# Optimization experiments

Hardware: AMD Instinct MI355X
Metric: run time of the kernel (lower is better)

Reference implementation:

```python
import jax, jax.numpy as jnp
import numpy as np

# Transformer config constants (from init_kwargs)
SRF = 3.0                 # spatial_receptive_field
SRF2 = SRF * SRF
ALPHA = 2.0
BETA = 8.0
GAMMA = 16.0
RES = jnp.array([0.5, 0.5, 0.5], dtype=jnp.float32)   # relative_positional_gresolution
N_BUCKETS = 2 * 8 + 1                                  # 2*beta + 1 = 17
MUL = jnp.array([N_BUCKETS ** 2, N_BUCKETS, 1], dtype=jnp.float32)  # [289,17,1]
SLICES_PER_ROT = 2


def setup_inputs() -> dict:
    key = jax.random.key(0)
    k1, k2 = jax.random.split(key)
    N = 3072
    # LiDAR-like point coordinates in a 10m cube; receptive field 3.0 makes radius filter selective
    xyz = jax.random.uniform(k1, (N, 3), dtype=jnp.float32) * 10.0
    # grid columns: [batch, block, gx, gy, gz]; values < 128 per the torch assert
    grid = jax.random.randint(k2, (N, 5), 0, 8, dtype=jnp.int32)
    return {"xyz": xyz, "grid": grid}


def _bucket_base(x):
    # from_dxyz_to_bucket_base, res.size(0)==3 branch
    x = x / RES
    x_abs = jnp.abs(x)
    log_ratio = jnp.log(jnp.maximum(x_abs, 1e-6) / ALPHA) / np.log(GAMMA / ALPHA)
    sup = jnp.minimum(jnp.round(ALPHA - (BETA - ALPHA) * log_ratio), BETA)
    sup = jnp.sign(x) * sup
    return BETA + jnp.where(x_abs <= ALPHA, jnp.round(x), sup)


def reference(xyz, grid):
    # no-kvp path of jit_compute_interactions, expressed as dense [N,N] pair masks
    batch = grid[:, 0]
    block = grid[:, 1]
    coords = grid[:, 2:]            # grid_look[:, 1:]

    # batch equality filter (meshgrid + batch==batch)
    batch_eq = batch[:, None] == batch[None, :]
    # causal block filter: block[iq] <= block[ik]
    block_le = block[:, None] <= block[None, :]

    # force_keep_neighbours: adjacent voxels within the same block
    coord_adj = jnp.max(jnp.abs(coords[:, None, :] - coords[None, :, :]), axis=-1) <= 1
    forcekeep = coord_adj & (block[:, None] == block[None, :])

    # coarse spatial hash on xy: ceil(xy / srf), neighbor cells only
    xy_coarse = jnp.ceil(xyz[:, :2] / SRF).astype(jnp.int32)
    keep_coarse = jnp.max(jnp.abs(xy_coarse[:, None, :] - xy_coarse[None, :, :]), axis=-1) <= 1

    # pairwise deltas (torch uses fp16 here; fp32 kept for numerical clarity) [N,N,3]
    dxyz = xyz[:, None, :] - xyz[None, :, :]
    keepr = jnp.sum(dxyz * dxyz, axis=-1) <= SRF2

    mask = batch_eq & block_le & (forcekeep | keep_coarse) & (forcekeep | keepr)

    dxyz_m = jnp.where(mask[..., None], dxyz, 0.0)

    # from_dxyz_to_bucket_mul: log-bucketize each axis, flatten via mul_buckets
    buckets = jnp.sum(MUL * _bucket_base(dxyz_m), axis=-1).astype(jnp.int32)
    buckets = jnp.where(mask, buckets, 0)

    # dscanid = scanid[ik] - scanid[iq], scanid = block // slices_per_rotation
    scanid = block // SLICES_PER_ROT
    dscanid = jnp.where(mask, scanid[None, :] - scanid[:, None], 0)

    return dxyz_m, buckets, dscanid, mask
```

## Files before the change

### kernel.cpp

```cpp
#include <hip/hip_runtime.h>
#include <cmath>


__device__ __forceinline__ float bucket_base(float v) {
    const float x  = v * 2.0f;
    const float xa = fabsf(x);
    if (xa <= 2.0f) {
        return 8.0f + rintf(x);
    }
    const float lr = logf(fmaxf(xa, 1e-6f) * 0.5f) / 2.0794415416798357f;
    const float sup = fminf(rintf(2.0f - 6.0f * lr), 8.0f);
    return 8.0f + ((x > 0.0f) ? sup : -sup);
}

template<int CN>
__device__ __forceinline__ void one_pair(
    const float* __restrict__ xyz, const int* __restrict__ grid,
    int Nrt, int p, float& dxm, float& dym, float& dzm)
{
#pragma clang fp contract(off)
    const int N = CN ? CN : Nrt;
    const int i = (int)((unsigned)p / (unsigned)N);
    const int j = p - i * N;
    const float xi = xyz[3*i+0], yi = xyz[3*i+1], zi = xyz[3*i+2];
    const float xj = xyz[3*j+0], yj = xyz[3*j+1], zj = xyz[3*j+2];
    const int bat_i = grid[5*i+0], blk_i = grid[5*i+1];
    const int c0i = grid[5*i+2], c1i = grid[5*i+3], c2i = grid[5*i+4];
    const int bat_j = grid[5*j+0], blk_j = grid[5*j+1];
    const int c0j = grid[5*j+2], c1j = grid[5*j+3], c2j = grid[5*j+4];
    const float dx = xi - xj, dy = yi - yj, dz = zi - zj;
    const bool batch_eq = (bat_i == bat_j);
    const bool block_le = (blk_i <= blk_j);
    const int  cadj = max(max(abs(c0i-c0j), abs(c1i-c1j)), abs(c2i-c2j));
    const bool forcekeep = (cadj <= 1) && (blk_i == blk_j);
    const int xci = (int)ceilf(xi/3.0f), yci = (int)ceilf(yi/3.0f);
    const int xcj = (int)ceilf(xj/3.0f), ycj = (int)ceilf(yj/3.0f);
    const bool keep_coarse = max(abs(xci-xcj), abs(yci-ycj)) <= 1;
    const float d2 = dx*dx + dy*dy + dz*dz;
    const bool keepr = (d2 <= 9.0f);
    const bool m = batch_eq && block_le &&
                   (forcekeep || keep_coarse) && (forcekeep || keepr);
    dxm = m ? dx : 0.0f; dym = m ? dy : 0.0f; dzm = m ? dz : 0.0f;
}

__device__ __forceinline__ void quad_mask(
    const float* __restrict__ xyz, const int* __restrict__ grid,
    int i, int j0,
    float dxm[4], float dym[4], float dzm[4], bool mk[4],
    int jblk[4], int& blk_i, bool& any)
{
#pragma clang fp contract(off)
    const float xi = xyz[3*i+0], yi = xyz[3*i+1], zi = xyz[3*i+2];
    const int bat_i = grid[5*i+0]; blk_i = grid[5*i+1];
    const int c0i = grid[5*i+2], c1i = grid[5*i+3], c2i = grid[5*i+4];
    const int xci = (int)ceilf(xi/3.0f), yci = (int)ceilf(yi/3.0f);

    const float4* pv = reinterpret_cast<const float4*>(xyz + (size_t)3 * j0);
    const float4 p0 = pv[0], p1 = pv[1], p2 = pv[2];
    const int4* gv = reinterpret_cast<const int4*>(grid + (size_t)5 * j0);
    const int4 g0 = gv[0], g1 = gv[1], g2 = gv[2], g3 = gv[3], g4 = gv[4];

    const float jx[4]  = {p0.x, p0.w, p1.z, p2.y};
    const float jy[4]  = {p0.y, p1.x, p1.w, p2.z};
    const float jz[4]  = {p0.z, p1.y, p2.x, p2.w};
    const int   jbat[4] = {g0.x, g1.y, g2.z, g3.w};
    const int   jb[4]   = {g0.y, g1.z, g2.w, g4.x};
    const int   jc0[4]  = {g0.z, g1.w, g3.x, g4.y};
    const int   jc1[4]  = {g0.w, g2.x, g3.y, g4.z};
    const int   jc2[4]  = {g1.x, g2.y, g3.z, g4.w};

    any = false;
#pragma unroll
    for (int k = 0; k < 4; ++k) {
        const float dx = xi - jx[k];
        const float dy = yi - jy[k];
        const float dz = zi - jz[k];
        const bool batch_eq = (bat_i == jbat[k]);
        const bool block_le = (blk_i <= jb[k]);
        const int  cadj = max(max(abs(c0i - jc0[k]), abs(c1i - jc1[k])),
                              abs(c2i - jc2[k]));
        const bool forcekeep = (cadj <= 1) && (blk_i == jb[k]);
        const int xcj = (int)ceilf(jx[k] / 3.0f);
        const int ycj = (int)ceilf(jy[k] / 3.0f);
        const bool keep_coarse = max(abs(xci - xcj), abs(yci - ycj)) <= 1;
        const float d2 = dx * dx + dy * dy + dz * dz;
        const bool keepr = (d2 <= 9.0f);
        const bool m = batch_eq && block_le &&
                       (forcekeep || keep_coarse) && (forcekeep || keepr);
        mk[k] = m; any |= m;
        jblk[k] = jb[k];
        dxm[k] = m ? dx : 0.0f;
        dym[k] = m ? dy : 0.0f;
        dzm[k] = m ? dz : 0.0f;
    }
}

template<int CN>
__global__ __launch_bounds__(256) void linear_kernel(
    const float* __restrict__ xyz, const int* __restrict__ grid,
    float* __restrict__ out, int Nrt)
{
    const int N = CN ? CN : Nrt;
    const unsigned NN = (unsigned)N * (unsigned)N;
    const unsigned t = blockIdx.x * blockDim.x + threadIdx.x;
    const unsigned e = t * 4u;
    if (e >= 6u * NN) return;
    float4* dst = reinterpret_cast<float4*>(out + (size_t)e);

    if (e < 3u * NN) {
        const unsigned c0 = e % 3u;
        const int p0 = (int)(e / 3u);
        float a0, a1, a2, b0, b1, b2;
        one_pair<CN>(xyz, grid, N, p0,     a0, a1, a2);
        one_pair<CN>(xyz, grid, N, p0 + 1, b0, b1, b2);
        float4 v;
        if (c0 == 0u)      v = make_float4(a0, a1, a2, b0);
        else if (c0 == 1u) v = make_float4(a1, a2, b0, b1);
        else               v = make_float4(a2, b0, b1, b2);
        *dst = v;
        return;
    }

    float dx[4], dy[4], dz[4];
    bool  mk[4];
    int   jblk[4], blk_i;
    bool  any;

    if (e < 4u * NN) {
        const int p = (int)(e - 3u * NN);
        const int i = (int)((unsigned)p / (unsigned)N);
        const int j0 = p - i * N;
        quad_mask(xyz, grid, i, j0, dx, dy, dz, mk, jblk, blk_i, any);
        if (__ballot(any ? 1 : 0) == 0ULL) {
            *dst = make_float4(0.0f, 0.0f, 0.0f, 0.0f);
            return;
        }
        float bf[4];
#pragma unroll
        for (int k = 0; k < 4; ++k) {
            if (mk[k]) {
                const float q0 = bucket_base(dx[k]);
                const float q1 = bucket_base(dy[k]);
                const float q2 = bucket_base(dz[k]);
                const float bsum = (289.0f * q0 + 17.0f * q1) + q2;
                bf[k] = (float)(int)bsum;
            } else {
                bf[k] = 0.0f;
            }
        }
        *dst = make_float4(bf[0], bf[1], bf[2], bf[3]);
    } else if (e < 5u * NN) {
        const int p = (int)(e - 4u * NN);
        const int i = (int)((unsigned)p / (unsigned)N);
        const int j0 = p - i * N;
        quad_mask(xyz, grid, i, j0, dx, dy, dz, mk, jblk, blk_i, any);
        const int scan_i = blk_i >> 1;
        float df[4];
#pragma unroll
        for (int k = 0; k < 4; ++k)
            df[k] = mk[k] ? (float)((jblk[k] >> 1) - scan_i) : 0.0f;
        *dst = make_float4(df[0], df[1], df[2], df[3]);
    } else {
        const int p = (int)(e - 5u * NN);
        const int i = (int)((unsigned)p / (unsigned)N);
        const int j0 = p - i * N;
        quad_mask(xyz, grid, i, j0, dx, dy, dz, mk, jblk, blk_i, any);
        float mf[4];
#pragma unroll
        for (int k = 0; k < 4; ++k)
            mf[k] = mk[k] ? 1.0f : 0.0f;
        *dst = make_float4(mf[0], mf[1], mf[2], mf[3]);
    }
}

extern "C" void kernel_launch(void* const* d_in, const int* in_sizes, int n_in,
                              void* d_out, int out_size, void* d_ws, size_t ws_size,
                              hipStream_t stream) {
    const float* xyz  = (const float*)d_in[0];
    const int*   grid = (const int*)d_in[1];
    float*       out  = (float*)d_out;
    const int N = in_sizes[0] / 3;

    const unsigned total  = 6u * (unsigned)N * (unsigned)N;
    const unsigned threads = (total + 3u) / 4u;
    const int BLOCK = 256;
    const unsigned blocks = (threads + BLOCK - 1) / BLOCK;
    if (N == 3072) {
        linear_kernel<3072><<<blocks, BLOCK, 0, stream>>>(xyz, grid, out, N);
    } else {
        linear_kernel<0><<<blocks, BLOCK, 0, stream>>>(xyz, grid, out, N);
    }
}
```

Baseline: 269.5 us.

## Split linear kernel into four per-output kernels on a 2D row grid

Replaces the single flat kernel, which decoded pair indices with integer divisions and had the dxyz section compute two pairs per thread, with four separate kernels, one per output tensor. Each launches on a 2D grid indexed by row i and a quad of j columns. The dxyz kernel now runs the vectorized quad mask once per four pairs and writes three float4s, dropping the per-element division and the duplicated mask work. The cost is four launches instead of one, and the code assumes N is divisible by 4 with no tail handling.

```diff
diff --git a/kernel.cpp b/kernel.cpp
--- a/kernel.cpp
+++ b/kernel.cpp
@@ -11,36 +11,6 @@
     const float lr = logf(fmaxf(xa, 1e-6f) * 0.5f) / 2.0794415416798357f;
     const float sup = fminf(rintf(2.0f - 6.0f * lr), 8.0f);
     return 8.0f + ((x > 0.0f) ? sup : -sup);
-}
-
-template<int CN>
-__device__ __forceinline__ void one_pair(
-    const float* __restrict__ xyz, const int* __restrict__ grid,
-    int Nrt, int p, float& dxm, float& dym, float& dzm)
-{
-#pragma clang fp contract(off)
-    const int N = CN ? CN : Nrt;
-    const int i = (int)((unsigned)p / (unsigned)N);
-    const int j = p - i * N;
-    const float xi = xyz[3*i+0], yi = xyz[3*i+1], zi = xyz[3*i+2];
-    const float xj = xyz[3*j+0], yj = xyz[3*j+1], zj = xyz[3*j+2];
-    const int bat_i = grid[5*i+0], blk_i = grid[5*i+1];
-    const int c0i = grid[5*i+2], c1i = grid[5*i+3], c2i = grid[5*i+4];
-    const int bat_j = grid[5*j+0], blk_j = grid[5*j+1];
-    const int c0j = grid[5*j+2], c1j = grid[5*j+3], c2j = grid[5*j+4];
-    const float dx = xi - xj, dy = yi - yj, dz = zi - zj;
-    const bool batch_eq = (bat_i == bat_j);
-    const bool block_le = (blk_i <= blk_j);
-    const int  cadj = max(max(abs(c0i-c0j), abs(c1i-c1j)), abs(c2i-c2j));
-    const bool forcekeep = (cadj <= 1) && (blk_i == blk_j);
-    const int xci = (int)ceilf(xi/3.0f), yci = (int)ceilf(yi/3.0f);
-    const int xcj = (int)ceilf(xj/3.0f), ycj = (int)ceilf(yj/3.0f);
-    const bool keep_coarse = max(abs(xci-xcj), abs(yci-ycj)) <= 1;
-    const float d2 = dx*dx + dy*dy + dz*dz;
-    const bool keepr = (d2 <= 9.0f);
-    const bool m = batch_eq && block_le &&
-                   (forcekeep || keep_coarse) && (forcekeep || keepr);
-    dxm = m ? dx : 0.0f; dym = m ? dy : 0.0f; dzm = m ? dz : 0.0f;
 }
 
 __device__ __forceinline__ void quad_mask(
@@ -95,82 +65,101 @@
     }
 }
 
-template<int CN>
-__global__ __launch_bounds__(256) void linear_kernel(
+__global__ __launch_bounds__(256) void k_dxyz(
     const float* __restrict__ xyz, const int* __restrict__ grid,
-    float* __restrict__ out, int Nrt)
+    float* __restrict__ dst, int N)
 {
-    const int N = CN ? CN : Nrt;
-    const unsigned NN = (unsigned)N * (unsigned)N;
-    const unsigned t = blockIdx.x * blockDim.x + threadIdx.x;
-    const unsigned e = t * 4u;
-    if (e >= 6u * NN) return;
-    float4* dst = reinterpret_cast<float4*>(out + (size_t)e);
+    const int jq = blockIdx.x * blockDim.x + threadIdx.x;
+    const int j0 = jq << 2;
+    const int i  = blockIdx.y;
+    if (j0 >= N) return;
 
-    if (e < 3u * NN) {
-        const unsigned c0 = e % 3u;
-        const int p0 = (int)(e / 3u);
-        float a0, a1, a2, b0, b1, b2;
-        one_pair<CN>(xyz, grid, N, p0,     a0, a1, a2);
-        one_pair<CN>(xyz, grid, N, p0 + 1, b0, b1, b2);
-        float4 v;
-        if (c0 == 0u)      v = make_float4(a0, a1, a2, b0);
-        else if (c0 == 1u) v = make_float4(a1, a2, b0, b1);
-        else               v = make_float4(a2, b0, b1, b2);
-        *dst = v;
+    float dx[4], dy[4], dz[4];
+    bool mk[4]; int jblk[4], blk_i; bool any;
+    quad_mask(xyz, grid, i, j0, dx, dy, dz, mk, jblk, blk_i, any);
+
+    const size_t base = ((size_t)i * (size_t)N + (size_t)j0) * 3;
+    float4* o = reinterpret_cast<float4*>(dst + base);
+    o[0] = make_float4(dx[0], dy[0], dz[0], dx[1]);
+    o[1] = make_float4(dy[1], dz[1], dx[2], dy[2]);
+    o[2] = make_float4(dz[2], dx[3], dy[3], dz[3]);
+}
+
+__global__ __launch_bounds__(256) void k_bkt(
+    const float* __restrict__ xyz, const int* __restrict__ grid,
+    float* __restrict__ dst, int N)
+{
+    const int jq = blockIdx.x * blockDim.x + threadIdx.x;
+    const int j0 = jq << 2;
+    const int i  = blockIdx.y;
+    if (j0 >= N) return;
+
+    float dx[4], dy[4], dz[4];
+    bool mk[4]; int jblk[4], blk_i; bool any;
+    quad_mask(xyz, grid, i, j0, dx, dy, dz, mk, jblk, blk_i, any);
+
+    float4* o = reinterpret_cast<float4*>(dst + (size_t)i * (size_t)N + (size_t)j0);
+    if (__ballot(any ? 1 : 0) == 0ULL) {
+        *o = make_float4(0.0f, 0.0f, 0.0f, 0.0f);
         return;
     }
+    float bf[4];
+#pragma unroll
+    for (int k = 0; k < 4; ++k) {
+        if (mk[k]) {
+            const float q0 = bucket_base(dx[k]);
+            const float q1 = bucket_base(dy[k]);
+            const float q2 = bucket_base(dz[k]);
+            const float bsum = (289.0f * q0 + 17.0f * q1) + q2;
+            bf[k] = (float)(int)bsum;
+        } else {
+            bf[k] = 0.0f;
+        }
+    }
+    *o = make_float4(bf[0], bf[1], bf[2], bf[3]);
+}
+
+__global__ __launch_bounds__(256) void k_dsc(
+    const float* __restrict__ xyz, const int* __restrict__ grid,
+    float* __restrict__ dst, int N)
+{
+    const int jq = blockIdx.x * blockDim.x + threadIdx.x;
+    const int j0 = jq << 2;
+    const int i  = blockIdx.y;
+    if (j0 >= N) return;
 
     float dx[4], dy[4], dz[4];
-    bool  mk[4];
-    int   jblk[4], blk_i;
-    bool  any;
+    bool mk[4]; int jblk[4], blk_i; bool any;
+    quad_mask(xyz, grid, i, j0, dx, dy, dz, mk, jblk, blk_i, any);
 
-    if (e < 4u * NN) {
-        const int p = (int)(e - 3u * NN);
-        const int i = (int)((unsigned)p / (unsigned)N);
-        const int j0 = p - i * N;
-        quad_mask(xyz, grid, i, j0, dx, dy, dz, mk, jblk, blk_i, any);
-        if (__ballot(any ? 1 : 0) == 0ULL) {
-            *dst = make_float4(0.0f, 0.0f, 0.0f, 0.0f);
-            return;
-        }
-        float bf[4];
+    const int scan_i = blk_i >> 1;
+    float df[4];
 #pragma unroll
-        for (int k = 0; k < 4; ++k) {
-            if (mk[k]) {
-                const float q0 = bucket_base(dx[k]);
-                const float q1 = bucket_base(dy[k]);
-                const float q2 = bucket_base(dz[k]);
-                const float bsum = (289.0f * q0 + 17.0f * q1) + q2;
-                bf[k] = (float)(int)bsum;
-            } else {
-                bf[k] = 0.0f;
-            }
-        }
-        *dst = make_float4(bf[0], bf[1], bf[2], bf[3]);
-    } else if (e < 5u * NN) {
-        const int p = (int)(e - 4u * NN);
-        const int i = (int)((unsigned)p / (unsigned)N);
-        const int j0 = p - i * N;
-        quad_mask(xyz, grid, i, j0, dx, dy, dz, mk, jblk, blk_i, any);
-        const int scan_i = blk_i >> 1;
-        float df[4];
+    for (int k = 0; k < 4; ++k)
+        df[k] = mk[k] ? (float)((jblk[k] >> 1) - scan_i) : 0.0f;
+    float4* o = reinterpret_cast<float4*>(dst + (size_t)i * (size_t)N + (size_t)j0);
+    *o = make_float4(df[0], df[1], df[2], df[3]);
+}
+
+__global__ __launch_bounds__(256) void k_msk(
+    const float* __restrict__ xyz, const int* __restrict__ grid,
+    float* __restrict__ dst, int N)
+{
+    const int jq = blockIdx.x * blockDim.x + threadIdx.x;
+    const int j0 = jq << 2;
+    const int i  = blockIdx.y;
+    if (j0 >= N) return;
+
+    float dx[4], dy[4], dz[4];
+    bool mk[4]; int jblk[4], blk_i; bool any;
+    quad_mask(xyz, grid, i, j0, dx, dy, dz, mk, jblk, blk_i, any);
+
+    float mf[4];
 #pragma unroll
-        for (int k = 0; k < 4; ++k)
-            df[k] = mk[k] ? (float)((jblk[k] >> 1) - scan_i) : 0.0f;
-        *dst = make_float4(df[0], df[1], df[2], df[3]);
-    } else {
-        const int p = (int)(e - 5u * NN);
-        const int i = (int)((unsigned)p / (unsigned)N);
-        const int j0 = p - i * N;
-        quad_mask(xyz, grid, i, j0, dx, dy, dz, mk, jblk, blk_i, any);
-        float mf[4];
-#pragma unroll
-        for (int k = 0; k < 4; ++k)
-            mf[k] = mk[k] ? 1.0f : 0.0f;
-        *dst = make_float4(mf[0], mf[1], mf[2], mf[3]);
-    }
+    for (int k = 0; k < 4; ++k)
+        mf[k] = mk[k] ? 1.0f : 0.0f;
+    float4* o = reinterpret_cast<float4*>(dst + (size_t)i * (size_t)N + (size_t)j0);
+    *o = make_float4(mf[0], mf[1], mf[2], mf[3]);
 }
 
 extern "C" void kernel_launch(void* const* d_in, const int* in_sizes, int n_in,
@@ -180,14 +169,15 @@
     const int*   grid = (const int*)d_in[1];
     float*       out  = (float*)d_out;
     const int N = in_sizes[0] / 3;
+    const size_t NN = (size_t)N * (size_t)N;
 
-    const unsigned total  = 6u * (unsigned)N * (unsigned)N;
-    const unsigned threads = (total + 3u) / 4u;
     const int BLOCK = 256;
-    const unsigned blocks = (threads + BLOCK - 1) / BLOCK;
-    if (N == 3072) {
-        linear_kernel<3072><<<blocks, BLOCK, 0, stream>>>(xyz, grid, out, N);
-    } else {
-        linear_kernel<0><<<blocks, BLOCK, 0, stream>>>(xyz, grid, out, N);
-    }
+    const int jquads = N / 4;
+    dim3 gdim((jquads + BLOCK - 1) / BLOCK, N, 1);
+    dim3 bdim(BLOCK, 1, 1);
+
+    k_dxyz<<<gdim, bdim, 0, stream>>>(xyz, grid, out,          N);
+    k_bkt <<<gdim, bdim, 0, stream>>>(xyz, grid, out + 3 * NN, N);
+    k_dsc <<<gdim, bdim, 0, stream>>>(xyz, grid, out + 4 * NN, N);
+    k_msk <<<gdim, bdim, 0, stream>>>(xyz, grid, out + 5 * NN, N);
 }
```

Result: slower. 279.6 us (+3.7%).
